# Kernel optimization log

Hardware: AMD Instinct MI355X
Metric: run time of the kernel (lower is better)

## Reference

```python
import jax, jax.numpy as jnp
import numpy as np

D = 1024
NHEAD = 16
HEAD_DIM = D // NHEAD


def setup_inputs() -> dict:
    key = jax.random.key(0)
    ks = jax.random.split(key, 7)
    B, L = 4, 2048
    q = jax.random.normal(ks[0], (B, L, D), dtype=jnp.float32)
    k = jax.random.normal(ks[1], (B, L, D), dtype=jnp.float32)
    v = jax.random.normal(ks[2], (B, L, D), dtype=jnp.float32)
    # packed QKV projection, as in nn.MultiheadAttention (in_proj_weight: [3d, d])
    scale = 1.0 / np.sqrt(D)
    in_proj_w = jax.random.uniform(ks[3], (3 * D, D), dtype=jnp.float32, minval=-scale, maxval=scale)
    in_proj_b = jnp.zeros((3 * D,), dtype=jnp.float32)
    out_w = jax.random.uniform(ks[4], (D, D), dtype=jnp.float32, minval=-scale, maxval=scale)
    out_b = jnp.zeros((D,), dtype=jnp.float32)
    return {"q": q, "k": k, "v": v, "in_proj_w": in_proj_w, "in_proj_b": in_proj_b,
            "out_w": out_w, "out_b": out_b}


def reference(q, k, v, in_proj_w, in_proj_b, out_w, out_b):
    # FP32 MHA, need_weights=True (average over heads), eval mode (dropout inactive).
    B, Lq, d = q.shape
    Lk = k.shape[1]
    # packed in-projection: rows [0:d] -> Q, [d:2d] -> K, [2d:3d] -> V
    qp = q @ in_proj_w[:d].T + in_proj_b[:d]
    kp = k @ in_proj_w[d:2 * d].T + in_proj_b[d:2 * d]
    vp = v @ in_proj_w[2 * d:].T + in_proj_b[2 * d:]
    # split heads: [B, H, L, hd]
    qp = qp.reshape(B, Lq, NHEAD, HEAD_DIM).transpose(0, 2, 1, 3)
    kp = kp.reshape(B, Lk, NHEAD, HEAD_DIM).transpose(0, 2, 1, 3)
    vp = vp.reshape(B, Lk, NHEAD, HEAD_DIM).transpose(0, 2, 1, 3)
    scores = jnp.einsum('bhqd,bhkd->bhqk', qp, kp) / jnp.sqrt(jnp.float32(HEAD_DIM))
    attn = jax.nn.softmax(scores, axis=-1)          # [B, H, Lq, Lk]
    ctx = jnp.einsum('bhqk,bhkd->bhqd', attn, vp)    # [B, H, Lq, hd]
    ctx = ctx.transpose(0, 2, 1, 3).reshape(B, Lq, d)
    out = ctx @ out_w.T + out_b                      # [B, Lq, d]
    weights = attn.mean(axis=1)                      # average over heads -> [B, Lq, Lk]
    return out, weights
```

## Files before the change

### kernel.cpp

```cpp
#include <hip/hip_runtime.h>
#include <hip/hip_bf16.h>

#define D_ 1024
#define NH 16
#define HD 64
#define B_ 4
#define L_ 2048
#define N_ (B_*L_)
#define BH_ (B_*NH)
#define QSCALE_ 0.18033688011112042f

typedef __bf16 bf16_t;
typedef __bf16 bf16x4 __attribute__((ext_vector_type(4)));
typedef __bf16 bf16x8 __attribute__((ext_vector_type(8)));
typedef float f32x4 __attribute__((ext_vector_type(4)));

typedef const __attribute__((address_space(1))) char gas_t;
typedef __attribute__((address_space(3))) char las_t;

__device__ __forceinline__ f32x4 mfma_bf16(bf16x8 a, bf16x8 b, f32x4 c) {
    return __builtin_amdgcn_mfma_f32_16x16x32_bf16(a, b, c, 0, 0, 0);
}

__device__ __forceinline__ bf16x8 cvt8_f32(const float* __restrict__ p) {
    const float4* p4 = reinterpret_cast<const float4*>(p);
    float4 a = p4[0], b = p4[1];
    bf16x8 r;
    r[0] = (bf16_t)a.x; r[1] = (bf16_t)a.y; r[2] = (bf16_t)a.z; r[3] = (bf16_t)a.w;
    r[4] = (bf16_t)b.x; r[5] = (bf16_t)b.y; r[6] = (bf16_t)b.z; r[7] = (bf16_t)b.w;
    return r;
}

__device__ __forceinline__ bf16x8 ld8_bf16(const bf16_t* __restrict__ p) {
    return *reinterpret_cast<const bf16x8*>(p);
}

__global__ __launch_bounds__(256) void k_cvt_all(
    const float* __restrict__ s0, const float* __restrict__ s1,
    const float* __restrict__ s2, const float* __restrict__ sw,
    const float* __restrict__ so,
    bf16_t* __restrict__ d0, bf16_t* __restrict__ d1, bf16_t* __restrict__ d2,
    bf16_t* __restrict__ dw, bf16_t* __restrict__ dow)
{
    const int n8  = N_ * D_ / 8;
    const int n8w = 3 * D_ * D_ / 8;
    const int n8o = D_ * D_ / 8;
    const int tot = 3 * n8 + n8w + n8o;
    int i = blockIdx.x * blockDim.x + threadIdx.x;
    int stride = gridDim.x * blockDim.x;
    for (; i < tot; i += stride) {
        const float* s; bf16_t* d; int off;
        if (i < 3 * n8) {
            int seg = i >> 20; off = i & (n8 - 1);
            s = (seg == 0) ? s0 : ((seg == 1) ? s1 : s2);
            d = (seg == 0) ? d0 : ((seg == 1) ? d1 : d2);
        } else if (i < 3 * n8 + n8w) {
            off = i - 3 * n8; s = sw; d = dw;
        } else {
            off = i - 3 * n8 - n8w; s = so; d = dow;
        }
        *reinterpret_cast<bf16x8*>(d + (size_t)off * 8) = cvt8_f32(s + (size_t)off * 8);
    }
}

__global__ __launch_bounds__(256) void k_gemm_qkv(
    const bf16_t* __restrict__ qb, const bf16_t* __restrict__ kb,
    const bf16_t* __restrict__ vb, const bf16_t* __restrict__ wb,
    const float* __restrict__ bias,
    bf16_t* __restrict__ qp, bf16_t* __restrict__ kp, bf16_t* __restrict__ vpT)
{
    __shared__ __align__(16) char lds[2][8192];
    int tid  = threadIdx.x;
    int lane = tid & 63, w = tid >> 6;
    int r = lane & 15, g = lane >> 4;
    int wr = w >> 1, wc = w & 1;

    int bid   = blockIdx.x;
    int xcd   = bid & 7;
    int seq   = bid >> 3;
    int sec   = seq >> 6;
    int inner = seq & 63;
    int tm  = xcd * 8 + (inner >> 3);
    int ctl = (inner & 7) * 128;

    const bf16_t* A = (sec == 0) ? qb : ((sec == 1) ? kb : vb);
    const bf16_t* Ab = A + (size_t)tm * 128 * 1024;
    const bf16_t* Bb = wb + (size_t)sec * D_ * D_ + (size_t)ctl * 1024;

    f32x4 z = {0.f, 0.f, 0.f, 0.f};
    f32x4 acc[4][4];
    #pragma unroll
    for (int m = 0; m < 4; ++m)
        #pragma unroll
        for (int n = 0; n < 4; ++n) acc[m][n] = z;

    for (int k0 = 0; k0 < 1024; k0 += 32) {
        #pragma unroll
        for (int i = 0; i < 2; ++i) {
            int o = i * 4096 + tid * 16;
            int row = o >> 6;
            int lchunk = ((o >> 4) & 3) ^ (row & 3);
            const bf16_t* gA = Ab + (size_t)row * 1024 + k0 + lchunk * 8;
            const bf16_t* gB = Bb + (size_t)row * 1024 + k0 + lchunk * 8;
            char* lpA = &lds[0][0] + i * 4096 + w * 1024;
            char* lpB = &lds[1][0] + i * 4096 + w * 1024;
            __builtin_amdgcn_global_load_lds((gas_t*)gA, (las_t*)lpA, 16, 0, 0);
            __builtin_amdgcn_global_load_lds((gas_t*)gB, (las_t*)lpB, 16, 0, 0);
        }
        __syncthreads();

        bf16x8 af[4], bf_[4];
        #pragma unroll
        for (int m = 0; m < 4; ++m) {
            int R = wr * 64 + m * 16 + r;
            af[m] = *reinterpret_cast<const bf16x8*>(
                &lds[0][0] + R * 64 + (((g ^ (R & 3)) << 4)));
        }
        #pragma unroll
        for (int n = 0; n < 4; ++n) {
            int R = wc * 64 + n * 16 + r;
            bf_[n] = *reinterpret_cast<const bf16x8*>(
                &lds[1][0] + R * 64 + (((g ^ (R & 3)) << 4)));
        }
        #pragma unroll
        for (int m = 0; m < 4; ++m)
            #pragma unroll
            for (int n = 0; n < 4; ++n)
                acc[m][n] = mfma_bf16(af[m], bf_[n], acc[m][n]);
        __syncthreads();
    }

    #pragma unroll
    for (int m = 0; m < 4; ++m)
        #pragma unroll
        for (int n = 0; n < 4; ++n)
            #pragma unroll
            for (int i = 0; i < 4; ++i) {
                int row = tm * 128 + wr * 64 + m * 16 + g * 4 + i;
                int col = ctl + wc * 64 + n * 16 + r;
                float val = acc[m][n][i] + bias[sec * 1024 + col];
                int bb = row >> 11, ln = row & 2047;
                int h = col >> 6, dd = col & 63;
                if (sec == 0)
                    qp[(((size_t)(bb * NH + h)) * L_ + ln) * HD + dd] =
                        (bf16_t)(val * QSCALE_);
                else if (sec == 1)
                    kp[(((size_t)(bb * NH + h)) * L_ + ln) * HD + dd] = (bf16_t)val;
                else
                    vpT[(((size_t)(bb * NH + h)) * HD + dd) * L_ + ln] = (bf16_t)val;
            }
}

__global__ __launch_bounds__(256) void k_gemm_out(
    const bf16_t* __restrict__ A, const bf16_t* __restrict__ Bm,
    const float* __restrict__ bias, float* __restrict__ dst)
{
    __shared__ __align__(16) char lds[2][8192];
    int tid  = threadIdx.x;
    int lane = tid & 63, w = tid >> 6;
    int r = lane & 15, g = lane >> 4;
    int wr = w >> 1, wc = w & 1;

    int bid = blockIdx.x;
    int swz = (bid & 7) * 64 + (bid >> 3);
    int tm = swz >> 3, tn = swz & 7;

    const bf16_t* Ab = A  + (size_t)tm * 128 * 1024;
    const bf16_t* Bb = Bm + (size_t)tn * 128 * 1024;

    f32x4 z = {0.f, 0.f, 0.f, 0.f};
    f32x4 acc[4][4];
    #pragma unroll
    for (int m = 0; m < 4; ++m)
        #pragma unroll
        for (int n = 0; n < 4; ++n) acc[m][n] = z;

    for (int k0 = 0; k0 < 1024; k0 += 32) {
        #pragma unroll
        for (int i = 0; i < 2; ++i) {
            int o = i * 4096 + tid * 16;
            int row = o >> 6;
            int lchunk = ((o >> 4) & 3) ^ (row & 3);
            const bf16_t* gA = Ab + (size_t)row * 1024 + k0 + lchunk * 8;
            const bf16_t* gB = Bb + (size_t)row * 1024 + k0 + lchunk * 8;
            char* lpA = &lds[0][0] + i * 4096 + w * 1024;
            char* lpB = &lds[1][0] + i * 4096 + w * 1024;
            __builtin_amdgcn_global_load_lds((gas_t*)gA, (las_t*)lpA, 16, 0, 0);
            __builtin_amdgcn_global_load_lds((gas_t*)gB, (las_t*)lpB, 16, 0, 0);
        }
        __syncthreads();

        bf16x8 af[4], bf_[4];
        #pragma unroll
        for (int m = 0; m < 4; ++m) {
            int R = wr * 64 + m * 16 + r;
            af[m] = *reinterpret_cast<const bf16x8*>(
                &lds[0][0] + R * 64 + (((g ^ (R & 3)) << 4)));
        }
        #pragma unroll
        for (int n = 0; n < 4; ++n) {
            int R = wc * 64 + n * 16 + r;
            bf_[n] = *reinterpret_cast<const bf16x8*>(
                &lds[1][0] + R * 64 + (((g ^ (R & 3)) << 4)));
        }
        #pragma unroll
        for (int m = 0; m < 4; ++m)
            #pragma unroll
            for (int n = 0; n < 4; ++n)
                acc[m][n] = mfma_bf16(af[m], bf_[n], acc[m][n]);
        __syncthreads();
    }

    #pragma unroll
    for (int m = 0; m < 4; ++m)
        #pragma unroll
        for (int n = 0; n < 4; ++n)
            #pragma unroll
            for (int i = 0; i < 4; ++i) {
                int row = tm * 128 + wr * 64 + m * 16 + g * 4 + i;
                int col = tn * 128 + wc * 64 + n * 16 + r;
                dst[(size_t)row * 1024 + col] = acc[m][n][i] + bias[col];
            }
}

__global__ __launch_bounds__(256, 4) void k_attn(
    const bf16_t* __restrict__ qp, const bf16_t* __restrict__ kp,
    const bf16_t* __restrict__ vpT,
    bf16_t* __restrict__ ctx, float* __restrict__ lInvOut)
{
    __shared__ __align__(16) char sK[8192];
    __shared__ __align__(16) char sV[8192];
    __shared__ __align__(16) char sP[4][4096];

    int tid  = threadIdx.x;
    int w    = tid >> 6;
    int lane = tid & 63;
    int r = lane & 15, g = lane >> 4;
    int bh = blockIdx.x & 63;
    int qg = blockIdx.x >> 6;
    int qbase = qg * 128 + w * 32;

    const bf16_t* qpb = qp  + (size_t)bh * L_ * HD;
    const bf16_t* kpb = kp  + (size_t)bh * L_ * HD;
    const bf16_t* vtb = vpT + (size_t)bh * HD * L_;

    bf16x8 bq[2][2];
    #pragma unroll
    for (int qt = 0; qt < 2; ++qt)
        #pragma unroll
        for (int ds = 0; ds < 2; ++ds)
            bq[qt][ds] = ld8_bf16(qpb + (size_t)(qbase + qt * 16 + r) * HD + ds * 32 + g * 8);

    bf16x8 ones;
    #pragma unroll
    for (int i = 0; i < 8; ++i) ones[i] = (bf16_t)1.0f;

    f32x4 z = {0.f, 0.f, 0.f, 0.f};
    f32x4 acc[2][4];
    #pragma unroll
    for (int qt = 0; qt < 2; ++qt)
        #pragma unroll
        for (int dt = 0; dt < 4; ++dt) acc[qt][dt] = z;
    f32x4 acc_l[2];
    acc_l[0] = z; acc_l[1] = z;

    char* Pw = &sP[w][0];

    int srow = tid >> 3;
    int slc  = (tid & 7) ^ (srow & 7);
    const bf16_t* gK0 = kpb + (size_t)srow * HD + slc * 8;
    const bf16_t* gV0 = vtb + (size_t)srow * L_ + slc * 8;

    for (int kt = 0; kt < 32; ++kt) {
        int k0 = kt * 64;
        const bf16_t* gK = gK0 + (size_t)k0 * HD;
        const bf16_t* gV = gV0 + k0;
        #pragma unroll
        for (int i = 0; i < 2; ++i) {
            __builtin_amdgcn_global_load_lds((gas_t*)(gK + (size_t)i * 32 * HD),
                (las_t*)(&sK[0] + i * 4096 + tid * 16), 16, 0, 0);
            __builtin_amdgcn_global_load_lds((gas_t*)(gV + (size_t)i * 32 * L_),
                (las_t*)(&sV[0] + i * 4096 + tid * 16), 16, 0, 0);
        }
        __syncthreads();

        f32x4 sT[4][2];
        __builtin_amdgcn_s_setprio(1);
        #pragma unroll
        for (int ktile = 0; ktile < 4; ++ktile) {
            bf16x8 a0 = *reinterpret_cast<const bf16x8*>(
                &sK[0] + (ktile * 16 + r) * 128 + (((g    ) ^ (r & 7)) << 4));
            bf16x8 a1 = *reinterpret_cast<const bf16x8*>(
                &sK[0] + (ktile * 16 + r) * 128 + (((4 + g) ^ (r & 7)) << 4));
            #pragma unroll
            for (int qt = 0; qt < 2; ++qt) {
                f32x4 t = mfma_bf16(a0, bq[qt][0], z);
                sT[ktile][qt] = mfma_bf16(a1, bq[qt][1], t);
            }
        }
        __builtin_amdgcn_s_setprio(0);

        #pragma unroll
        for (int qt = 0; qt < 2; ++qt) {
            #pragma unroll
            for (int ktile = 0; ktile < 4; ++ktile) {
                bf16x4 pw;
                #pragma unroll
                for (int i = 0; i < 4; ++i)
                    pw[i] = (bf16_t)__builtin_amdgcn_exp2f(sT[ktile][qt][i]);
                *reinterpret_cast<bf16x4*>(Pw + (qt * 16 + r) * 128 +
                    (((2 * ktile + (g >> 1)) ^ (r & 7)) << 4) + ((g & 1) << 3)) = pw;
            }
        }

        bf16x8 pa[2][2];
        #pragma unroll
        for (int qt = 0; qt < 2; ++qt)
            #pragma unroll
            for (int ks = 0; ks < 2; ++ks)
                pa[qt][ks] = *reinterpret_cast<const bf16x8*>(
                    Pw + (qt * 16 + r) * 128 + (((4 * ks + g) ^ (r & 7)) << 4));
        __builtin_amdgcn_s_setprio(1);
        #pragma unroll
        for (int qt = 0; qt < 2; ++qt) {
            acc_l[qt] = mfma_bf16(pa[qt][0], ones, acc_l[qt]);
            acc_l[qt] = mfma_bf16(pa[qt][1], ones, acc_l[qt]);
        }
        #pragma unroll
        for (int dt = 0; dt < 4; ++dt)
            #pragma unroll
            for (int ks = 0; ks < 2; ++ks) {
                bf16x8 bv = *reinterpret_cast<const bf16x8*>(
                    &sV[0] + (dt * 16 + r) * 128 + (((4 * ks + g) ^ (r & 7)) << 4));
                acc[0][dt] = mfma_bf16(pa[0][ks], bv, acc[0][dt]);
                acc[1][dt] = mfma_bf16(pa[1][ks], bv, acc[1][dt]);
            }
        __builtin_amdgcn_s_setprio(0);

        __syncthreads();
    }

    int bb = bh >> 4, h = bh & 15;
    #pragma unroll
    for (int qt = 0; qt < 2; ++qt) {
        float lq[4];
        #pragma unroll
        for (int i = 0; i < 4; ++i) lq[i] = 1.0f / acc_l[qt][i];
        #pragma unroll
        for (int i = 0; i < 4; ++i) {
            int q = qbase + qt * 16 + 4 * g + i;
            #pragma unroll
            for (int dt = 0; dt < 4; ++dt) {
                float val = acc[qt][dt][i] * lq[i];
                ctx[(((size_t)(bb * L_ + q)) * NH + h) * HD + dt * 16 + r] = (bf16_t)val;
            }
        }
        if (r == 0) {
            #pragma unroll
            for (int i = 0; i < 4; ++i) {
                int q = qbase + qt * 16 + 4 * g + i;
                lInvOut[(size_t)bh * L_ + q] = lq[i];
            }
        }
    }
}

__global__ __launch_bounds__(256, 2) void k_weights(
    const bf16_t* __restrict__ qp, const bf16_t* __restrict__ kp,
    const float* __restrict__ lInv, float* __restrict__ wout)
{
    __shared__ __align__(16) char sQ[2][16384];
    __shared__ __align__(16) char sKt[2][16384];
    __shared__ __align__(16) float sLi[16][128];

    int tid  = threadIdx.x;
    int w    = tid >> 6;
    int lane = tid & 63;
    int r = lane & 15, g = lane >> 4;
    int wr = w >> 1, wc = w & 1;

    int wgid = (blockIdx.x & 7) * 128 + (blockIdx.x >> 3);
    int chunk = wgid >> 7;
    int b  = chunk >> 1;
    int qh = chunk & 1;
    int rem = wgid & 127;
    int qt = qh * 8 + (rem >> 4);
    int kt = rem & 15;
    int q0 = qt * 128, k0 = kt * 128;

    #pragma unroll
    for (int i = 0; i < 2; ++i) {
        int idx = i * 256 + tid;
        int h   = idx >> 5;
        int off = (idx & 31) * 4;
        const float* gl = lInv + ((size_t)(b * NH + h) * L_ + q0 + off);
        __builtin_amdgcn_global_load_lds((gas_t*)gl,
            (las_t*)((char*)&sLi[0][0] + i * 4096 + w * 1024), 16, 0, 0);
    }

    auto stage_qk = [&](int buf, int h) {
        const bf16_t* Qh = qp + ((size_t)(b * NH + h) * L_ + q0) * HD;
        const bf16_t* Kh = kp + ((size_t)(b * NH + h) * L_ + k0) * HD;
        #pragma unroll
        for (int i = 0; i < 4; ++i) {
            int idx = i * 256 + tid;
            int row = idx >> 3;
            int lc  = (idx & 7) ^ (row & 7);
            const bf16_t* gQ = Qh + (size_t)row * HD + lc * 8;
            const bf16_t* gK = Kh + (size_t)row * HD + lc * 8;
            __builtin_amdgcn_global_load_lds((gas_t*)gQ,
                (las_t*)(&sQ[buf][0]  + i * 4096 + w * 1024), 16, 0, 0);
            __builtin_amdgcn_global_load_lds((gas_t*)gK,
                (las_t*)(&sKt[buf][0] + i * 4096 + w * 1024), 16, 0, 0);
        }
    };

    float acc[4][4][4] = {};
    f32x4 z = {0.f, 0.f, 0.f, 0.f};

    stage_qk(0, 0);
    __syncthreads();
    int buf = 0;

    for (int h = 0; h < NH; ++h) {
        if (h + 1 < NH) stage_qk(buf ^ 1, h + 1);

        const char* Qb = &sQ[buf][0];
        const char* Kb = &sKt[buf][0];

        bf16x8 bfrag[4][2];
        #pragma unroll
        for (int nf = 0; nf < 4; ++nf) {
            int R = wc * 64 + nf * 16 + r;
            bfrag[nf][0] = *reinterpret_cast<const bf16x8*>(
                Kb + R * 128 + (((g    ) ^ (R & 7)) << 4));
            bfrag[nf][1] = *reinterpret_cast<const bf16x8*>(
                Kb + R * 128 + (((4 + g) ^ (R & 7)) << 4));
        }
        #pragma unroll
        for (int mf = 0; mf < 4; ++mf) {
            int R = wr * 64 + mf * 16 + r;
            bf16x8 af0 = *reinterpret_cast<const bf16x8*>(
                Qb + R * 128 + (((g    ) ^ (R & 7)) << 4));
            bf16x8 af1 = *reinterpret_cast<const bf16x8*>(
                Qb + R * 128 + (((4 + g) ^ (R & 7)) << 4));
            int qrow = wr * 64 + mf * 16 + g * 4;
            f32x4 liv = *reinterpret_cast<const f32x4*>(&sLi[h][qrow]);
            #pragma unroll
            for (int nf = 0; nf < 4; ++nf) {
                f32x4 t = mfma_bf16(af0, bfrag[nf][0], z);
                t = mfma_bf16(af1, bfrag[nf][1], t);
                #pragma unroll
                for (int i = 0; i < 4; ++i)
                    acc[mf][nf][i] += __builtin_amdgcn_exp2f(t[i]) * liv[i];
            }
        }
        __syncthreads();
        buf ^= 1;
    }

    const float inv_h = 1.0f / (float)NH;
    #pragma unroll
    for (int mf = 0; mf < 4; ++mf)
        #pragma unroll
        for (int nf = 0; nf < 4; ++nf)
            #pragma unroll
            for (int i = 0; i < 4; ++i) {
                int qidx = q0 + wr * 64 + mf * 16 + g * 4 + i;
                int kidx = k0 + wc * 64 + nf * 16 + r;
                wout[((size_t)(b * L_ + qidx)) * L_ + kidx] = acc[mf][nf][i] * inv_h;
            }
}

extern "C" void kernel_launch(void* const* d_in, const int* in_sizes, int n_in,
                              void* d_out, int out_size, void* d_ws, size_t ws_size,
                              hipStream_t stream) {
    const float* q     = (const float*)d_in[0];
    const float* k     = (const float*)d_in[1];
    const float* v     = (const float*)d_in[2];
    const float* in_w  = (const float*)d_in[3];
    const float* in_b  = (const float*)d_in[4];
    const float* out_w = (const float*)d_in[5];
    const float* out_b = (const float*)d_in[6];

    char* ws = (char*)d_ws;
    bf16_t* xb   = (bf16_t*)(ws);
    bf16_t* wb   = (bf16_t*)(ws + ((size_t)48 << 20));
    bf16_t* owb  = (bf16_t*)(ws + ((size_t)54 << 20));
    bf16_t* qp   = (bf16_t*)(ws + ((size_t)56 << 20));
    bf16_t* kp   = (bf16_t*)(ws + ((size_t)72 << 20));
    bf16_t* vpT  = (bf16_t*)(ws + ((size_t)88 << 20));
    bf16_t* ctx  = (bf16_t*)(ws + ((size_t)104 << 20));
    float*  lBuf = (float*)(ws + ((size_t)120 << 20));

    bf16_t* qb = xb;
    bf16_t* kb = xb + (size_t)N_ * D_;
    bf16_t* vb = xb + (size_t)2 * N_ * D_;

    float* outp = (float*)d_out;
    float* wout = outp + (size_t)N_ * D_;

    k_cvt_all<<<2048, 256, 0, stream>>>(q, k, v, in_w, out_w, qb, kb, vb, wb, owb);

    k_gemm_qkv<<<1536, 256, 0, stream>>>(qb, kb, vb, wb, in_b, qp, kp, vpT);

    k_attn   <<<1024, 256, 0, stream>>>(qp, kp, vpT, ctx, lBuf);
    k_weights<<<1024, 256, 0, stream>>>(qp, kp, lBuf, wout);

    k_gemm_out<<<512, 256, 0, stream>>>(ctx, owb, out_b, outp);
}
```

Measured before the change: 274.3 us.

## Fuse fp32-to-bf16 activation conversion into QKV GEMM and double-buffer GEMM loads

The standalone conversion of the q/k/v activations to bf16 is removed. The QKV GEMM now stages fp32 activation tiles directly into LDS and converts them to bf16 when reading MFMA fragments. This avoids writing and re-reading 48MB of bf16 intermediates. Both GEMMs also gain double-buffered LDS staging so the next k-slice loads while the current one computes, and their block-to-tile swizzles are changed. The cost is doubled activation LDS traffic, extra conversion ALU inside the GEMM inner loop, and more LDS per block.

Result: slower. 301.1 us (+9.8%).

```diff
diff --git a/kernel.cpp b/kernel.cpp
--- a/kernel.cpp
+++ b/kernel.cpp
@@ -35,56 +35,46 @@
     return *reinterpret_cast<const bf16x8*>(p);
 }
 
-__global__ __launch_bounds__(256) void k_cvt_all(
-    const float* __restrict__ s0, const float* __restrict__ s1,
-    const float* __restrict__ s2, const float* __restrict__ sw,
-    const float* __restrict__ so,
-    bf16_t* __restrict__ d0, bf16_t* __restrict__ d1, bf16_t* __restrict__ d2,
+__global__ __launch_bounds__(256) void k_cvt_w(
+    const float* __restrict__ sw, const float* __restrict__ so,
     bf16_t* __restrict__ dw, bf16_t* __restrict__ dow)
 {
-    const int n8  = N_ * D_ / 8;
     const int n8w = 3 * D_ * D_ / 8;
     const int n8o = D_ * D_ / 8;
-    const int tot = 3 * n8 + n8w + n8o;
     int i = blockIdx.x * blockDim.x + threadIdx.x;
     int stride = gridDim.x * blockDim.x;
-    for (; i < tot; i += stride) {
-        const float* s; bf16_t* d; int off;
-        if (i < 3 * n8) {
-            int seg = i >> 20; off = i & (n8 - 1);
-            s = (seg == 0) ? s0 : ((seg == 1) ? s1 : s2);
-            d = (seg == 0) ? d0 : ((seg == 1) ? d1 : d2);
-        } else if (i < 3 * n8 + n8w) {
-            off = i - 3 * n8; s = sw; d = dw;
-        } else {
-            off = i - 3 * n8 - n8w; s = so; d = dow;
-        }
-        *reinterpret_cast<bf16x8*>(d + (size_t)off * 8) = cvt8_f32(s + (size_t)off * 8);
+    for (; i < n8w + n8o; i += stride) {
+        if (i < n8w)
+            *reinterpret_cast<bf16x8*>(dw + (size_t)i * 8) = cvt8_f32(sw + (size_t)i * 8);
+        else {
+            int j = i - n8w;
+            *reinterpret_cast<bf16x8*>(dow + (size_t)j * 8) = cvt8_f32(so + (size_t)j * 8);
+        }
     }
 }
 
 __global__ __launch_bounds__(256) void k_gemm_qkv(
-    const bf16_t* __restrict__ qb, const bf16_t* __restrict__ kb,
-    const bf16_t* __restrict__ vb, const bf16_t* __restrict__ wb,
+    const float* __restrict__ qf, const float* __restrict__ kf,
+    const float* __restrict__ vf, const bf16_t* __restrict__ wb,
     const float* __restrict__ bias,
     bf16_t* __restrict__ qp, bf16_t* __restrict__ kp, bf16_t* __restrict__ vpT)
 {
-    __shared__ __align__(16) char lds[2][8192];
+    __shared__ __align__(16) char ldsA[2][16384];
+    __shared__ __align__(16) char ldsB[2][8192];
     int tid  = threadIdx.x;
     int lane = tid & 63, w = tid >> 6;
     int r = lane & 15, g = lane >> 4;
     int wr = w >> 1, wc = w & 1;
 
-    int bid   = blockIdx.x;
-    int xcd   = bid & 7;
-    int seq   = bid >> 3;
-    int sec   = seq >> 6;
-    int inner = seq & 63;
-    int tm  = xcd * 8 + (inner >> 3);
-    int ctl = (inner & 7) * 128;
-
-    const bf16_t* A = (sec == 0) ? qb : ((sec == 1) ? kb : vb);
-    const bf16_t* Ab = A + (size_t)tm * 128 * 1024;
+    int bid = blockIdx.x;
+    int xcd = bid & 7;
+    int seq = bid >> 3;
+    int sec = seq >> 6;
+    int tm  = seq & 63;
+    int ctl = xcd * 128;
+
+    const float* A = (sec == 0) ? qf : ((sec == 1) ? kf : vf);
+    const float* Ab = A + (size_t)tm * 128 * 1024;
     const bf16_t* Bb = wb + (size_t)sec * D_ * D_ + (size_t)ctl * 1024;
 
     f32x4 z = {0.f, 0.f, 0.f, 0.f};
@@ -94,40 +84,64 @@
         #pragma unroll
         for (int n = 0; n < 4; ++n) acc[m][n] = z;
 
+    auto stage = [&](int buf, int k0) {
+        #pragma unroll
+        for (int i = 0; i < 4; ++i) {
+            int idx = i * 256 + tid;
+            int row = idx >> 3;
+            int lc  = (idx & 7) ^ (row & 7);
+            const float* gA = Ab + (size_t)row * 1024 + k0 + lc * 4;
+            __builtin_amdgcn_global_load_lds((gas_t*)gA,
+                (las_t*)(&ldsA[buf][0] + idx * 16), 16, 0, 0);
+        }
+        #pragma unroll
+        for (int i = 0; i < 2; ++i) {
+            int idx = i * 256 + tid;
+            int row = idx >> 2;
+            int lc  = (idx & 3) ^ (row & 3);
+            const bf16_t* gB = Bb + (size_t)row * 1024 + k0 + lc * 8;
+            __builtin_amdgcn_global_load_lds((gas_t*)gB,
+                (las_t*)(&ldsB[buf][0] + idx * 16), 16, 0, 0);
+        }
+    };
+
+    stage(0, 0);
+    __syncthreads();
+    int buf = 0;
+
     for (int k0 = 0; k0 < 1024; k0 += 32) {
-        #pragma unroll
-        for (int i = 0; i < 2; ++i) {
-            int o = i * 4096 + tid * 16;
-            int row = o >> 6;
-            int lchunk = ((o >> 4) & 3) ^ (row & 3);
-            const bf16_t* gA = Ab + (size_t)row * 1024 + k0 + lchunk * 8;
-            const bf16_t* gB = Bb + (size_t)row * 1024 + k0 + lchunk * 8;
-            char* lpA = &lds[0][0] + i * 4096 + w * 1024;
-            char* lpB = &lds[1][0] + i * 4096 + w * 1024;
-            __builtin_amdgcn_global_load_lds((gas_t*)gA, (las_t*)lpA, 16, 0, 0);
-            __builtin_amdgcn_global_load_lds((gas_t*)gB, (las_t*)lpB, 16, 0, 0);
-        }
-        __syncthreads();
+        if (k0 + 32 < 1024) stage(buf ^ 1, k0 + 32);
+
+        const char* Ablds = &ldsA[buf][0];
+        const char* Bblds = &ldsB[buf][0];
 
         bf16x8 af[4], bf_[4];
         #pragma unroll
         for (int m = 0; m < 4; ++m) {
             int R = wr * 64 + m * 16 + r;
-            af[m] = *reinterpret_cast<const bf16x8*>(
-                &lds[0][0] + R * 64 + (((g ^ (R & 3)) << 4)));
+            f32x4 lo = *reinterpret_cast<const f32x4*>(
+                Ablds + R * 128 + ((((2 * g)    ) ^ (R & 7)) << 4));
+            f32x4 hi = *reinterpret_cast<const f32x4*>(
+                Ablds + R * 128 + ((((2 * g) + 1) ^ (R & 7)) << 4));
+            bf16x8 a;
+            #pragma unroll
+            for (int j = 0; j < 4; ++j) { a[j] = (bf16_t)lo[j]; a[4 + j] = (bf16_t)hi[j]; }
+            af[m] = a;
         }
         #pragma unroll
         for (int n = 0; n < 4; ++n) {
             int R = wc * 64 + n * 16 + r;
             bf_[n] = *reinterpret_cast<const bf16x8*>(
-                &lds[1][0] + R * 64 + (((g ^ (R & 3)) << 4)));
+                Bblds + R * 64 + (((g ^ (R & 3)) << 4)));
         }
         #pragma unroll
         for (int m = 0; m < 4; ++m)
             #pragma unroll
             for (int n = 0; n < 4; ++n)
                 acc[m][n] = mfma_bf16(af[m], bf_[n], acc[m][n]);
+
         __syncthreads();
+        buf ^= 1;
     }
 
     #pragma unroll
@@ -155,15 +169,15 @@
     const bf16_t* __restrict__ A, const bf16_t* __restrict__ Bm,
     const float* __restrict__ bias, float* __restrict__ dst)
 {
-    __shared__ __align__(16) char lds[2][8192];
+    __shared__ __align__(16) char ldsA[2][8192];
+    __shared__ __align__(16) char ldsB[2][8192];
     int tid  = threadIdx.x;
     int lane = tid & 63, w = tid >> 6;
     int r = lane & 15, g = lane >> 4;
     int wr = w >> 1, wc = w & 1;
 
     int bid = blockIdx.x;
-    int swz = (bid & 7) * 64 + (bid >> 3);
-    int tm = swz >> 3, tn = swz & 7;
+    int tm = bid >> 3, tn = bid & 7;
 
     const bf16_t* Ab = A  + (size_t)tm * 128 * 1024;
     const bf16_t* Bb = Bm + (size_t)tn * 128 * 1024;
@@ -175,40 +189,49 @@
         #pragma unroll
         for (int n = 0; n < 4; ++n) acc[m][n] = z;
 
+    auto stage = [&](int buf, int k0) {
+        #pragma unroll
+        for (int i = 0; i < 2; ++i) {
+            int idx = i * 256 + tid;
+            int row = idx >> 2;
+            int lc  = (idx & 3) ^ (row & 3);
+            const bf16_t* gA = Ab + (size_t)row * 1024 + k0 + lc * 8;
+            const bf16_t* gB = Bb + (size_t)row * 1024 + k0 + lc * 8;
+            __builtin_amdgcn_global_load_lds((gas_t*)gA,
+                (las_t*)(&ldsA[buf][0] + idx * 16), 16, 0, 0);
+            __builtin_amdgcn_global_load_lds((gas_t*)gB,
+                (las_t*)(&ldsB[buf][0] + idx * 16), 16, 0, 0);
+        }
+    };
+
+    stage(0, 0);
+    __syncthreads();
+    int buf = 0;
+
     for (int k0 = 0; k0 < 1024; k0 += 32) {
-        #pragma unroll
-        for (int i = 0; i < 2; ++i) {
-            int o = i * 4096 + tid * 16;
-            int row = o >> 6;
-            int lchunk = ((o >> 4) & 3) ^ (row & 3);
-            const bf16_t* gA = Ab + (size_t)row * 1024 + k0 + lchunk * 8;
-            const bf16_t* gB = Bb + (size_t)row * 1024 + k0 + lchunk * 8;
-            char* lpA = &lds[0][0] + i * 4096 + w * 1024;
-            char* lpB = &lds[1][0] + i * 4096 + w * 1024;
-            __builtin_amdgcn_global_load_lds((gas_t*)gA, (las_t*)lpA, 16, 0, 0);
-            __builtin_amdgcn_global_load_lds((gas_t*)gB, (las_t*)lpB, 16, 0, 0);
-        }
-        __syncthreads();
+        if (k0 + 32 < 1024) stage(buf ^ 1, k0 + 32);
 
         bf16x8 af[4], bf_[4];
         #pragma unroll
         for (int m = 0; m < 4; ++m) {
             int R = wr * 64 + m * 16 + r;
             af[m] = *reinterpret_cast<const bf16x8*>(
-                &lds[0][0] + R * 64 + (((g ^ (R & 3)) << 4)));
+                &ldsA[buf][0] + R * 64 + (((g ^ (R & 3)) << 4)));
         }
         #pragma unroll
         for (int n = 0; n < 4; ++n) {
             int R = wc * 64 + n * 16 + r;
             bf_[n] = *reinterpret_cast<const bf16x8*>(
-                &lds[1][0] + R * 64 + (((g ^ (R & 3)) << 4)));
+                &ldsB[buf][0] + R * 64 + (((g ^ (R & 3)) << 4)));
         }
         #pragma unroll
         for (int m = 0; m < 4; ++m)
             #pragma unroll
             for (int n = 0; n < 4; ++n)
                 acc[m][n] = mfma_bf16(af[m], bf_[n], acc[m][n]);
+
         __syncthreads();
+        buf ^= 1;
     }
 
     #pragma unroll
@@ -484,7 +507,6 @@
     const float* out_b = (const float*)d_in[6];
 
     char* ws = (char*)d_ws;
-    bf16_t* xb   = (bf16_t*)(ws);
     bf16_t* wb   = (bf16_t*)(ws + ((size_t)48 << 20));
     bf16_t* owb  = (bf16_t*)(ws + ((size_t)54 << 20));
     bf16_t* qp   = (bf16_t*)(ws + ((size_t)56 << 20));
@@ -493,16 +515,12 @@
     bf16_t* ctx  = (bf16_t*)(ws + ((size_t)104 << 20));
     float*  lBuf = (float*)(ws + ((size_t)120 << 20));
 
-    bf16_t* qb = xb;
-    bf16_t* kb = xb + (size_t)N_ * D_;
-    bf16_t* vb = xb + (size_t)2 * N_ * D_;
-
     float* outp = (float*)d_out;
     float* wout = outp + (size_t)N_ * D_;
 
-    k_cvt_all<<<2048, 256, 0, stream>>>(q, k, v, in_w, out_w, qb, kb, vb, wb, owb);
-
-    k_gemm_qkv<<<1536, 256, 0, stream>>>(qb, kb, vb, wb, in_b, qp, kp, vpT);
+    k_cvt_w<<<512, 256, 0, stream>>>(in_w, out_w, wb, owb);
+
+    k_gemm_qkv<<<1536, 256, 0, stream>>>(q, k, v, wb, in_b, qp, kp, vpT);
 
     k_attn   <<<1024, 256, 0, stream>>>(qp, kp, vpT, ctx, lBuf);
     k_weights<<<1024, 256, 0, stream>>>(qp, kp, lBuf, wout);
```
